# Optimization experiments

Measured on AMD Instinct MI355X. Metric: run time of the kernel, lower is better.

The kernel has to match this reference:

```python
import jax, jax.numpy as jnp
import numpy as np

N_ANCHORS = 200000
TOPK = 4096          # pre-NMS top-k (standard detector practice, fixed output shape)
CONF_T = 0.5
IOU_T = 0.6


def setup_inputs() -> dict:
    key = jax.random.key(0)
    k1, k2, k3 = jax.random.split(key, 3)
    # build valid xyxy boxes: random centers in a 1024x1024 image, sizes 4..128
    cxcy = jax.random.uniform(k1, (1, N_ANCHORS, 2), minval=0.0, maxval=1024.0)
    wh = jax.random.uniform(k2, (1, N_ANCHORS, 2), minval=4.0, maxval=128.0)
    boxes = jnp.concatenate([cxcy - wh / 2, cxcy + wh / 2], axis=-1)  # [1,N,4]
    confs = jax.random.uniform(k3, (1, N_ANCHORS))                    # [1,N]
    return {"boxes": boxes, "confs": confs}


def _pairwise_iou(b):
    # b: [K,4] xyxy -> iou: [K,K]
    area = jnp.clip(b[:, 2] - b[:, 0], 0.0) * jnp.clip(b[:, 3] - b[:, 1], 0.0)
    lt = jnp.maximum(b[:, None, :2], b[None, :, :2])
    rb = jnp.minimum(b[:, None, 2:], b[None, :, 2:])
    wh = jnp.clip(rb - lt, 0.0)
    inter = wh[..., 0] * wh[..., 1]
    return inter / (area[:, None] + area[None, :] - inter + 1e-9)


def reference(boxes, confs):
    b = boxes[0]          # [N,4] single batch (module is single-batch single-class)
    c = confs[0]          # [N]
    # confidence threshold mask; invalid scores pushed below any valid score
    scores = jnp.where(c >= CONF_T, c, -1.0)
    top_scores, idx = jax.lax.top_k(scores, TOPK)   # sorted descending
    top_boxes = b[idx]                              # [K,4]
    iou = _pairwise_iou(top_boxes)                  # [K,K]
    valid_k = top_scores >= CONF_T

    # greedy sequential NMS over score-sorted candidates
    def body(i, state):
        keep, sup = state
        is_keep = jnp.logical_not(sup[i])
        keep = keep.at[i].set(is_keep)
        sup = sup | (is_keep & (iou[i] > IOU_T))
        return (keep, sup)

    keep0 = jnp.zeros((TOPK,), dtype=bool)
    keep, _ = jax.lax.fori_loop(0, TOPK, body, (keep0, jnp.logical_not(valid_k)))

    # [K,5] = x1,y1,x2,y2,conf ; suppressed rows zeroed (fixed output shape)
    out = jnp.concatenate([top_boxes, top_scores[:, None]], axis=-1)
    return jnp.where(keep[:, None], out, 0.0)
```

## Files before the change

### kernel.cpp

```cpp
#include <hip/hip_runtime.h>

#define NTOP   4096
#define SORTN  8192
#define CONF_T 0.5f
#define IOU_T  0.6f

#define HIST_OFF   0
#define CUT_OFF    8192
#define CNT_OFF    8196
#define COMP_OFF   16384
#define MEMSET_BYTES 81920
#define KEYS_OFF   131072
#define TB_OFF     2097152
#define TC_OFF     2162688
#define VALID_OFF  2179072
#define KEEP_OFF   2179584
#define MASK_OFF   4194304

typedef unsigned long long u64;
typedef unsigned int u32;

__global__ void k_keys(const float* __restrict__ confs, u64* __restrict__ keys,
                       u32* __restrict__ hist, int n) {
    int i = blockIdx.x * 256 + threadIdx.x;
    if (i >= n) return;
    float s = confs[i];
    if (s >= CONF_T) {
        u32 u = __float_as_uint(s);
        keys[i] = ((u64)u << 32) | (u32)(~i);
        int bin = (int)(u >> 12) - 0x3F000;
        bin = bin < 0 ? 0 : (bin > 2047 ? 2047 : bin);
        atomicAdd(&hist[bin], 1u);
    } else {
        keys[i] = 0ull;
    }
}

__global__ __launch_bounds__(256) void k_findcut(const u32* __restrict__ hist,
                                                 int* __restrict__ cut) {
    __shared__ u32 ch[256];
    int t = threadIdx.x;
    u32 h[8]; u32 s = 0;
#pragma unroll
    for (int k = 0; k < 8; ++k) { h[k] = hist[t * 8 + k]; s += h[k]; }
    ch[t] = s;
    __syncthreads();
    for (int off = 1; off < 256; off <<= 1) {
        u32 v = ch[t];
        u32 add = (t + off < 256) ? ch[t + off] : 0u;
        __syncthreads();
        ch[t] = v + add;
        __syncthreads();
    }
    u32 incl = ch[t];
    u32 above = incl - s;
    if (above < NTOP && incl >= NTOP) {
        u32 cum = above; int c = 0;
        for (int k = 7; k >= 0; --k) {
            cum += h[k];
            if (cum >= NTOP) { c = t * 8 + k; break; }
        }
        *cut = c;
    }
    if (t == 0 && ch[0] < NTOP) *cut = 0;
}

__global__ void k_compact(const u64* __restrict__ keys, const int* __restrict__ cut,
                          u64* __restrict__ comp, u32* __restrict__ counter, int n) {
    int i = blockIdx.x * 256 + threadIdx.x;
    if (i >= n) return;
    u64 key = keys[i];
    if (!key) return;
    int bin = (int)(u32)(key >> 44) - 0x3F000;
    bin = bin < 0 ? 0 : (bin > 2047 ? 2047 : bin);
    if (bin >= *cut) {
        u32 p = atomicAdd(counter, 1u);
        if (p < SORTN) comp[p] = key;
    }
}

__global__ __launch_bounds__(1024) void k_sort(u64* __restrict__ comp) {
    __shared__ u64 sm[SORTN];
    int t = threadIdx.x;
    for (int i = t; i < SORTN; i += 1024) sm[i] = comp[i];
    __syncthreads();
    for (int k = 2; k <= SORTN; k <<= 1) {
        for (int j = k >> 1; j > 0; j >>= 1) {
            for (int i = t; i < SORTN; i += 1024) {
                int ixj = i ^ j;
                if (ixj > i) {
                    u64 a = sm[i], b = sm[ixj];
                    bool sw = ((i & k) == 0) ? (a < b) : (a > b);
                    if (sw) { sm[i] = b; sm[ixj] = a; }
                }
            }
            __syncthreads();
        }
    }
    for (int i = t; i < SORTN; i += 1024) comp[i] = sm[i];
}

__global__ void k_gather(const u64* __restrict__ skeys, const float4* __restrict__ boxes,
                         float4* __restrict__ tb, float* __restrict__ tc,
                         u64* __restrict__ validmask) {
    int k = blockIdx.x * 256 + threadIdx.x;
    u64 key = skeys[k];
    float score = __uint_as_float((u32)(key >> 32));
    bool valid = (key != 0ull) && (score >= CONF_T);
    float4 b = make_float4(0.f, 0.f, 0.f, 0.f);
    if (valid) {
        u32 idx = ~(u32)(key & 0xFFFFFFFFull);
        b = boxes[idx];
    }
    tb[k] = b;
    tc[k] = score;
    u64 bal = __ballot(valid);
    if ((threadIdx.x & 63) == 0) validmask[k >> 6] = bal;
}

__global__ __launch_bounds__(256) void k_mask(const float4* __restrict__ tb,
                                              u64* __restrict__ mask) {
    __shared__ float4 cb[64];
    __shared__ float  ca[64];
    int w = blockIdx.x;
    int t = threadIdx.x;
    if (t < 64) {
        float4 b = tb[w * 64 + t];
        cb[t] = b;
        ca[t] = fmaxf(b.z - b.x, 0.f) * fmaxf(b.w - b.y, 0.f);
    }
    __syncthreads();
    int row = blockIdx.y * 256 + t;
    float4 rb = tb[row];
    float ra = fmaxf(rb.z - rb.x, 0.f) * fmaxf(rb.w - rb.y, 0.f);
    u64 m = 0;
#pragma unroll 8
    for (int j = 0; j < 64; ++j) {
        float4 c = cb[j];
        float lx = fmaxf(rb.x, c.x), ly = fmaxf(rb.y, c.y);
        float rx = fminf(rb.z, c.z), ry = fminf(rb.w, c.w);
        float iw = fmaxf(rx - lx, 0.f), ih = fmaxf(ry - ly, 0.f);
        float inter = iw * ih;
        float iou = inter / (ra + ca[j] - inter + 1e-9f);
        if (iou > IOU_T) m |= (1ull << j);
    }
    mask[(size_t)row * 64 + w] = m;
}

__global__ __launch_bounds__(64) void k_nms(const u64* __restrict__ mask,
                                            const u64* __restrict__ validmask,
                                            u64* __restrict__ keep) {
    __shared__ u64 dw[NTOP];
    int lane = threadIdx.x;
    for (int i = lane; i < NTOP; i += 64) dw[i] = mask[(size_t)i * 64 + (i >> 6)];
    u64 mysup = ~validmask[lane];
    __syncthreads();

    u64 mykeep = 0;
    u64 pf[16];
#pragma unroll
    for (int d = 0; d < 16; ++d) pf[d] = mask[(size_t)d * 64 + lane];

    for (int w = 0; w < 64; ++w) {
        u64 cur = __shfl(mysup, w);
        u64 blockkeep = 0;
        for (int sub = 0; sub < 64; sub += 16) {
#pragma unroll
            for (int d = 0; d < 16; ++d) {
                int i = (w << 6) + sub + d;
                int nxt = (i + 16 < NTOP) ? (i + 16) : i;
                u64 rowv = pf[d];
                pf[d] = mask[(size_t)nxt * 64 + lane];
                u64 dwv = dw[i];
                int bit = sub + d;
                bool is_keep = ((cur >> bit) & 1ull) == 0ull;
                if (is_keep) {
                    cur |= dwv;
                    mysup |= rowv;
                    blockkeep |= (1ull << bit);
                }
            }
        }
        if (lane == w) mykeep = blockkeep;
    }
    keep[lane] = mykeep;
}

__global__ void k_out(const float4* __restrict__ tb, const float* __restrict__ tc,
                      const u64* __restrict__ keep, float* __restrict__ out) {
    int k = blockIdx.x * 256 + threadIdx.x;
    bool kp = (keep[k >> 6] >> (k & 63)) & 1ull;
    float4 b = tb[k];
    float c = tc[k];
    float* o = out + (size_t)k * 5;
    o[0] = kp ? b.x : 0.f;
    o[1] = kp ? b.y : 0.f;
    o[2] = kp ? b.z : 0.f;
    o[3] = kp ? b.w : 0.f;
    o[4] = kp ? c : 0.f;
}

extern "C" void kernel_launch(void* const* d_in, const int* in_sizes, int n_in,
                              void* d_out, int out_size, void* d_ws, size_t ws_size,
                              hipStream_t stream) {
    const float4* boxes = (const float4*)d_in[0];
    const float*  confs = (const float*)d_in[1];
    float* out = (float*)d_out;
    char* ws = (char*)d_ws;
    int n = in_sizes[1];

    u32* hist    = (u32*)(ws + HIST_OFF);
    int* cut     = (int*)(ws + CUT_OFF);
    u32* counter = (u32*)(ws + CNT_OFF);
    u64* comp    = (u64*)(ws + COMP_OFF);
    u64* keys    = (u64*)(ws + KEYS_OFF);
    float4* tb   = (float4*)(ws + TB_OFF);
    float*  tc   = (float*)(ws + TC_OFF);
    u64* validm  = (u64*)(ws + VALID_OFF);
    u64* keep    = (u64*)(ws + KEEP_OFF);
    u64* mask    = (u64*)(ws + MASK_OFF);

    hipMemsetAsync(ws, 0, MEMSET_BYTES, stream);
    k_keys<<<(n + 255) / 256, 256, 0, stream>>>(confs, keys, hist, n);
    k_findcut<<<1, 256, 0, stream>>>(hist, cut);
    k_compact<<<(n + 255) / 256, 256, 0, stream>>>(keys, cut, comp, counter, n);
    k_sort<<<1, 1024, 0, stream>>>(comp);
    k_gather<<<16, 256, 0, stream>>>(comp, boxes, tb, tc, validm);
    k_mask<<<dim3(64, 16), 256, 0, stream>>>(tb, mask);
    k_nms<<<1, 64, 0, stream>>>(mask, validm, keep);
    k_out<<<16, 256, 0, stream>>>(tb, tc, keep, out);
}
```

Measured before the change: 504.5 us.

## Fuse gather into sort kernel and use readlane for NMS diagonal words

The sort kernel now gathers boxes, scores and the valid mask directly from shared memory, which removes the separate gather launch and the write-back of sorted keys to global memory. The NMS kernel drops its shared-memory diagonal table and instead pulls each diagonal word from the prefetched row register with readlane, so the upfront strided load and the barrier go away. It also deepens the row prefetch from 16 to 32 and makes the keep update branchless with masks. The deeper register prefetch and full unrolling raise register pressure in the single-wave serial NMS loop.

After: 439.7 us. 1.15x faster.

```diff
diff --git a/kernel.cpp b/kernel.cpp
--- a/kernel.cpp
+++ b/kernel.cpp
@@ -79,7 +79,11 @@
     }
 }
 
-__global__ __launch_bounds__(1024) void k_sort(u64* __restrict__ comp) {
+__global__ __launch_bounds__(1024) void k_sort(const u64* __restrict__ comp,
+                                               const float4* __restrict__ boxes,
+                                               float4* __restrict__ tb,
+                                               float* __restrict__ tc,
+                                               u64* __restrict__ validmask) {
     __shared__ u64 sm[SORTN];
     int t = threadIdx.x;
     for (int i = t; i < SORTN; i += 1024) sm[i] = comp[i];
@@ -97,25 +101,21 @@
             __syncthreads();
         }
     }
-    for (int i = t; i < SORTN; i += 1024) comp[i] = sm[i];
-}
-
-__global__ void k_gather(const u64* __restrict__ skeys, const float4* __restrict__ boxes,
-                         float4* __restrict__ tb, float* __restrict__ tc,
-                         u64* __restrict__ validmask) {
-    int k = blockIdx.x * 256 + threadIdx.x;
-    u64 key = skeys[k];
-    float score = __uint_as_float((u32)(key >> 32));
-    bool valid = (key != 0ull) && (score >= CONF_T);
-    float4 b = make_float4(0.f, 0.f, 0.f, 0.f);
-    if (valid) {
-        u32 idx = ~(u32)(key & 0xFFFFFFFFull);
-        b = boxes[idx];
-    }
-    tb[k] = b;
-    tc[k] = score;
-    u64 bal = __ballot(valid);
-    if ((threadIdx.x & 63) == 0) validmask[k >> 6] = bal;
+    for (int base = 0; base < NTOP; base += 1024) {
+        int k = base + t;
+        u64 key = sm[k];
+        float score = __uint_as_float((u32)(key >> 32));
+        bool valid = (key != 0ull) && (score >= CONF_T);
+        float4 b = make_float4(0.f, 0.f, 0.f, 0.f);
+        if (valid) {
+            u32 idx = ~(u32)(key & 0xFFFFFFFFull);
+            b = boxes[idx];
+        }
+        tb[k] = b;
+        tc[k] = score;
+        u64 bal = __ballot(valid);
+        if ((t & 63) == 0) validmask[k >> 6] = bal;
+    }
 }
 
 __global__ __launch_bounds__(256) void k_mask(const float4* __restrict__ tb,
@@ -150,35 +150,36 @@
 __global__ __launch_bounds__(64) void k_nms(const u64* __restrict__ mask,
                                             const u64* __restrict__ validmask,
                                             u64* __restrict__ keep) {
-    __shared__ u64 dw[NTOP];
     int lane = threadIdx.x;
-    for (int i = lane; i < NTOP; i += 64) dw[i] = mask[(size_t)i * 64 + (i >> 6)];
     u64 mysup = ~validmask[lane];
-    __syncthreads();
-
     u64 mykeep = 0;
-    u64 pf[16];
-#pragma unroll
-    for (int d = 0; d < 16; ++d) pf[d] = mask[(size_t)d * 64 + lane];
+
+    u64 pf[32];
+#pragma unroll
+    for (int d = 0; d < 32; ++d) pf[d] = mask[(size_t)d * 64 + lane];
 
     for (int w = 0; w < 64; ++w) {
-        u64 cur = __shfl(mysup, w);
+        u32 clo = (u32)__builtin_amdgcn_readlane((int)(u32)mysup, w);
+        u32 chi = (u32)__builtin_amdgcn_readlane((int)(u32)(mysup >> 32), w);
+        u64 cur = ((u64)chi << 32) | clo;
         u64 blockkeep = 0;
-        for (int sub = 0; sub < 64; sub += 16) {
-#pragma unroll
-            for (int d = 0; d < 16; ++d) {
+#pragma unroll
+        for (int sub = 0; sub < 64; sub += 32) {
+#pragma unroll
+            for (int d = 0; d < 32; ++d) {
                 int i = (w << 6) + sub + d;
-                int nxt = (i + 16 < NTOP) ? (i + 16) : i;
+                int nxt = i + 32; if (nxt >= NTOP) nxt = i;
                 u64 rowv = pf[d];
                 pf[d] = mask[(size_t)nxt * 64 + lane];
-                u64 dwv = dw[i];
-                int bit = sub + d;
+                u32 dlo = (u32)__builtin_amdgcn_readlane((int)(u32)rowv, w);
+                u32 dhi = (u32)__builtin_amdgcn_readlane((int)(u32)(rowv >> 32), w);
+                u64 dwv = ((u64)dhi << 32) | dlo;
+                const int bit = sub + d;
                 bool is_keep = ((cur >> bit) & 1ull) == 0ull;
-                if (is_keep) {
-                    cur |= dwv;
-                    mysup |= rowv;
-                    blockkeep |= (1ull << bit);
-                }
+                u64 m = is_keep ? ~0ull : 0ull;
+                cur |= dwv & m;
+                mysup |= rowv & m;
+                blockkeep |= is_keep ? (1ull << bit) : 0ull;
             }
         }
         if (lane == w) mykeep = blockkeep;
@@ -224,8 +225,7 @@
     k_keys<<<(n + 255) / 256, 256, 0, stream>>>(confs, keys, hist, n);
     k_findcut<<<1, 256, 0, stream>>>(hist, cut);
     k_compact<<<(n + 255) / 256, 256, 0, stream>>>(keys, cut, comp, counter, n);
-    k_sort<<<1, 1024, 0, stream>>>(comp);
-    k_gather<<<16, 256, 0, stream>>>(comp, boxes, tb, tc, validm);
+    k_sort<<<1, 1024, 0, stream>>>(comp, boxes, tb, tc, validm);
     k_mask<<<dim3(64, 16), 256, 0, stream>>>(tb, mask);
     k_nms<<<1, 64, 0, stream>>>(mask, validm, keep);
     k_out<<<16, 256, 0, stream>>>(tb, tc, keep, out);
```
